# Performance work log

Hardware: AMD Instinct MI355X
Metric: run time of the kernel (lower is better)

Reference implementation:

```python
import jax, jax.numpy as jnp
import numpy as np

ALPHA = 0.2  # LeakyReLU negative slope
MASK_VAL = -9e15


def gat_layer(h, W, a, adj):
    # h: (b, n, f_in); W: (H, f_in, d); a: (H, 2d, 1); adj: (n, n)
    Wh = jnp.einsum('bni,hid->bhnd', h, W)          # (b, H, n, d)
    d = W.shape[-1]
    a1 = a[:, :d, 0]                                # (H, d) -> source term
    a2 = a[:, d:, 0]                                # (H, d) -> target term
    f1 = jnp.einsum('bhnd,hd->bhn', Wh, a1)
    f2 = jnp.einsum('bhnd,hd->bhn', Wh, a2)
    e = jax.nn.leaky_relu(f1[..., :, None] + f2[..., None, :], ALPHA)  # (b, H, n, n)
    e = jnp.where(adj > 0, e, MASK_VAL)
    att = jax.nn.softmax(e, axis=-1)
    out = jnp.einsum('bhij,bhjd->bhid', att, Wh)    # (b, H, n, d)
    b, H, n, dd = out.shape
    # concat heads along feature dim (matches torch.cat(head_outputs, dim=2))
    return jnp.transpose(out, (0, 2, 1, 3)).reshape(b, n, H * dd)


def setup_inputs() -> dict:
    key = jax.random.key(0)
    ks = jax.random.split(key, 8)
    B, N = 131072, 9
    HID, OUT, HEADS = 96, 48, 3
    hd1 = HID // HEADS   # 32
    hd2 = OUT // HEADS   # 16

    def xavier(k, shape, gain=1.414):
        fan_in, fan_out = shape[-2], shape[-1]
        lim = gain * np.sqrt(6.0 / (fan_in + fan_out))
        return jax.random.uniform(k, shape, jnp.float32, -lim, lim)

    obs = jax.random.normal(ks[0], (B, N), dtype=jnp.float32)
    adj = jnp.ones((N, N), dtype=jnp.float32)
    W1 = xavier(ks[1], (HEADS, 1, hd1))
    a1 = xavier(ks[2], (HEADS, 2 * hd1, 1))
    W2 = xavier(ks[3], (HEADS, HID, hd2))
    a2 = xavier(ks[4], (HEADS, 2 * hd2, 1))
    lim = np.sqrt(1.0 / OUT)
    Wp1 = jax.random.uniform(ks[5], (OUT, OUT // 2), jnp.float32, -lim, lim)
    bp1 = jnp.zeros((OUT // 2,), jnp.float32)
    lim2 = np.sqrt(1.0 / (OUT // 2))
    Wp2 = jax.random.uniform(ks[6], (OUT // 2, 1), jnp.float32, -lim2, lim2)
    bp2 = jnp.zeros((1,), jnp.float32)
    return {"obs": obs, "adj": adj, "W1": W1, "a1": a1, "W2": W2, "a2": a2,
            "Wp1": Wp1, "bp1": bp1, "Wp2": Wp2, "bp2": bp2}


def reference(obs, adj, W1, a1, W2, a2, Wp1, bp1, Wp2, bp2):
    h = obs[..., None]                       # (b, n, 1)
    h = jax.nn.elu(gat_layer(h, W1, a1, adj))
    h = gat_layer(h, W2, a2, adj)            # (b, n, output_dim)
    # attention pooling over nodes
    scores = jnp.tanh(h @ Wp1 + bp1) @ Wp2 + bp2   # (b, n, 1)
    w = jax.nn.softmax(scores, axis=1)
    return jnp.sum(w * h, axis=1)            # (b, output_dim)
```

## Files before the change

kernel.cpp:

```cpp
#include <hip/hip_runtime.h>
#include <math.h>

typedef _Float16 h16;
typedef _Float16 v2h __attribute__((ext_vector_type(2)));

#define ALPHA 0.2f
#define MASKV -9000000000000000.0f

constexpr int GSCR = 268;
constexpr int O_S  = 0;
constexpr int O_F1 = 28;
constexpr int O_F2 = 56;
constexpr int O_U  = 92;

#if defined(__has_builtin)
#  if __has_builtin(__builtin_amdgcn_fdot2)
#    define FDOT2(a,b,c) __builtin_amdgcn_fdot2((a),(b),(c),false)
#  endif
#endif
#ifndef FDOT2
__device__ __forceinline__ float fdot2_sw(v2h a, v2h b, float c) {
    return c + (float)a.x*(float)b.x + (float)a.y*(float)b.y;
}
#  define FDOT2(a,b,c) fdot2_sw((a),(b),(c))
#endif

union U4 { float4 f; v2h h[4]; };
union U2 { float2 f; v2h h[2]; };
union U1 { float  f; v2h h;    };

#define WAVE_SYNC() asm volatile("s_waitcnt lgkmcnt(0)" ::: "memory")

__device__ __forceinline__ float fast_rcp(float x) { return __builtin_amdgcn_rcpf(x); }
__device__ __forceinline__ float tanh_fast(float x) {
    float e = __expf(x + x);
    return 1.f - 2.f * fast_rcp(e + 1.f);
}

__global__ void prep_kernel(const float* __restrict__ W2, const float* __restrict__ Wp1,
                            h16* __restrict__ ws) {
    int t = blockIdx.x * 256 + threadIdx.x;
    if (t < 48 * 96) {
        int c = t / 96, i = t - c * 96;
        int h = c >> 4, d = c & 15;
        ws[t] = (h16)W2[(h * 96 + i) * 16 + d];
    } else if (t < 48 * 96 + 576) {
        int t2 = t - 48 * 96;
        int k = t2 / 24, s = t2 - k * 24;
        int l = s / 3, kp = s - 3 * l;
        int clo = l + 16 * kp, chi = clo + 8;
        ws[4608 + 2 * t2]     = (h16)Wp1[clo * 24 + k];
        ws[4608 + 2 * t2 + 1] = (h16)Wp1[chi * 24 + k];
    }
}

__global__ __launch_bounds__(128, 4) void gnn_gat_kernel(
    const float* __restrict__ obs, const float* __restrict__ adj,
    const float* __restrict__ W1,  const float* __restrict__ a1,
    const float* __restrict__ a2,  const float* __restrict__ bp1,
    const float* __restrict__ Wp2, const h16* __restrict__ ws,
    float* __restrict__ out, int B)
{
    __shared__ float sW1[96];
    __shared__ float sC12[6];
    __shared__ unsigned sRb[9];
    __shared__ __align__(16) float smem[16 * GSCR];

    const int tid = threadIdx.x;
    if (tid < 96) sW1[tid] = W1[tid];
    if (tid < 9) {
        unsigned u = 0;
        for (int j = 0; j < 9; ++j)
            u |= (adj[tid * 9 + j] > 0.f ? 1u : 0u) << j;
        sRb[tid] = u;
    }
    if (tid < 6) {
        int gg = tid >> 1, w = tid & 1;
        float s = 0.f;
        for (int d = 0; d < 32; ++d)
            s += W1[gg * 32 + d] * a1[gg * 64 + w * 32 + d];
        sC12[tid] = s;
    }
    __syncthreads();

    const int wv = tid >> 6, lane = tid & 63;
    const int q = lane >> 3, l8 = lane & 7;
    float* g = smem + (wv * 8 + q) * GSCR;
    float4* hUf4 = (float4*)(g + O_U);
    float4* h2f4 = (float4*)g;
    const float4* wsf4 = (const float4*)ws;

    const int slots = gridDim.x * 16;
    for (int b = (blockIdx.x * 2 + wv) * 8 + q; b < B; b += slots) {
        float o_r[9];
        #pragma unroll
        for (int j = 0; j < 9; ++j) o_r[j] = obs[(size_t)b * 9 + j];
        g[O_F1 + l8] = obs[(size_t)b * 9 + l8];
        if (l8 == 0) g[O_F1 + 8] = obs[(size_t)b * 9 + 8];
        WAVE_SYNC();

        #pragma unroll
        for (int it = 0; it < 4; ++it) {
            int t = l8 + 8 * it;
            if (t < 27) {
                int gg = (t >= 18) ? 2 : (t >= 9 ? 1 : 0);
                int n = t - 9 * gg;
                float f1 = sC12[2 * gg] * g[O_F1 + n];
                float c2 = sC12[2 * gg + 1];
                unsigned rbits = sRb[n];
                float e[9], m = -3.0e38f;
                #pragma unroll
                for (int j = 0; j < 9; ++j) {
                    float x = f1 + c2 * o_r[j];
                    x = x > 0.f ? x : ALPHA * x;
                    x = ((rbits >> j) & 1) ? x : MASKV;
                    e[j] = x; m = fmaxf(m, x);
                }
                float sum = 0.f, sw = 0.f;
                #pragma unroll
                for (int j = 0; j < 9; ++j) {
                    float p = __expf(e[j] - m);
                    sum += p; sw += p * o_r[j];
                }
                g[O_S + t] = sw * fast_rcp(sum);
            }
        }
        WAVE_SYNC();

        float acc[9][6];
        #pragma unroll
        for (int n = 0; n < 9; ++n)
            #pragma unroll
            for (int k = 0; k < 6; ++k) acc[n][k] = 0.f;

        for (int p = 0; p < 3; ++p) {
            #pragma unroll
            for (int it = 0; it < 5; ++it) {
                int t = l8 + 8 * it;
                if (t < 36) {
                    int n = t >> 2, ib = t & 3;
                    int i0 = 32 * p + 8 * ib;
                    float sv = g[O_S + p * 9 + n];
                    float4 wa = *(const float4*)&sW1[i0];
                    float4 wb = *(const float4*)&sW1[i0 + 4];
                    float v0 = sv * wa.x, v1 = sv * wa.y, v2 = sv * wa.z, v3 = sv * wa.w;
                    float v4 = sv * wb.x, v5 = sv * wb.y, v6 = sv * wb.z, v7 = sv * wb.w;
                    v0 = v0 > 0.f ? v0 : __expf(v0) - 1.f;
                    v1 = v1 > 0.f ? v1 : __expf(v1) - 1.f;
                    v2 = v2 > 0.f ? v2 : __expf(v2) - 1.f;
                    v3 = v3 > 0.f ? v3 : __expf(v3) - 1.f;
                    v4 = v4 > 0.f ? v4 : __expf(v4) - 1.f;
                    v5 = v5 > 0.f ? v5 : __expf(v5) - 1.f;
                    v6 = v6 > 0.f ? v6 : __expf(v6) - 1.f;
                    v7 = v7 > 0.f ? v7 : __expf(v7) - 1.f;
                    U4 u;
                    u.h[0] = (v2h){(h16)v0, (h16)v1};
                    u.h[1] = (v2h){(h16)v2, (h16)v3};
                    u.h[2] = (v2h){(h16)v4, (h16)v5};
                    u.h[3] = (v2h){(h16)v6, (h16)v7};
                    hUf4[n * 4 + ib] = u.f;
                }
            }
            WAVE_SYNC();

            #pragma unroll
            for (int ib = 0; ib < 4; ++ib) {
                U4 w[6];
                #pragma unroll
                for (int k = 0; k < 6; ++k)
                    w[k].f = wsf4[(l8 + 8 * k) * 12 + p * 4 + ib];
                #pragma unroll
                for (int n = 0; n < 9; ++n) {
                    U4 hh; hh.f = hUf4[n * 4 + ib];
                    #pragma unroll
                    for (int k = 0; k < 6; ++k) {
                        float a = acc[n][k];
                        a = FDOT2(hh.h[0], w[k].h[0], a);
                        a = FDOT2(hh.h[1], w[k].h[1], a);
                        a = FDOT2(hh.h[2], w[k].h[2], a);
                        a = FDOT2(hh.h[3], w[k].h[3], a);
                        acc[n][k] = a;
                    }
                }
            }
            WAVE_SYNC();
        }

        #pragma unroll
        for (int h = 0; h < 3; ++h) {
            float aa0 = a2[h * 32 + l8];
            float aa1 = a2[h * 32 + 8 + l8];
            float ab0 = a2[h * 32 + 16 + l8];
            float ab1 = a2[h * 32 + 24 + l8];
            #pragma unroll
            for (int n = 0; n < 9; ++n) {
                float v1 = acc[n][2 * h] * aa0 + acc[n][2 * h + 1] * aa1;
                float v2 = acc[n][2 * h] * ab0 + acc[n][2 * h + 1] * ab1;
                v1 += __shfl_xor(v1, 1, 8); v1 += __shfl_xor(v1, 2, 8); v1 += __shfl_xor(v1, 4, 8);
                v2 += __shfl_xor(v2, 1, 8); v2 += __shfl_xor(v2, 2, 8); v2 += __shfl_xor(v2, 4, 8);
                if (((h * 9 + n) & 7) == l8) {
                    g[O_F1 + h * 9 + n]  = v1;
                    g[O_F2 + h * 10 + n] = v2;
                }
            }
        }
        WAVE_SYNC();

        #pragma unroll
        for (int it = 0; it < 4; ++it) {
            int t = l8 + 8 * it;
            if (t < 27) {
                int h = (t >= 18) ? 2 : (t >= 9 ? 1 : 0);
                int i = t - 9 * h;
                float f1i = g[O_F1 + t];
                unsigned rbits = sRb[i];
                float e[9], m = -3.0e38f;
                #pragma unroll
                for (int j = 0; j < 9; ++j) {
                    float x = f1i + g[O_F2 + h * 10 + j];
                    x = x > 0.f ? x : ALPHA * x;
                    x = ((rbits >> j) & 1) ? x : MASKV;
                    e[j] = x; m = fmaxf(m, x);
                }
                float p[9], sum = 0.f;
                #pragma unroll
                for (int j = 0; j < 9; ++j) { p[j] = __expf(e[j] - m); sum += p[j]; }
                float r = fast_rcp(sum);
                char* row = (char*)(g + O_U) + t * 24;
                U2 u01, u23; U1 u4;
                u01.h[0] = (v2h){(h16)(p[0] * r), (h16)(p[1] * r)};
                u01.h[1] = (v2h){(h16)(p[2] * r), (h16)(p[3] * r)};
                u23.h[0] = (v2h){(h16)(p[4] * r), (h16)(p[5] * r)};
                u23.h[1] = (v2h){(h16)(p[6] * r), (h16)(p[7] * r)};
                u4.h     = (v2h){(h16)(p[8] * r), (h16)0.f};
                *(float2*)(row)      = u01.f;
                *(float2*)(row + 8)  = u23.f;
                *(float*)(row + 16)  = u4.f;
            }
        }
        WAVE_SYNC();

        #pragma unroll
        for (int h = 0; h < 3; ++h) {
            float t0[9], t1[9];
            #pragma unroll
            for (int i = 0; i < 9; ++i) {
                const char* row = (const char*)(g + O_U) + (h * 9 + i) * 24;
                U2 a01, a23; U1 a4;
                a01.f = *(const float2*)row;
                a23.f = *(const float2*)(row + 8);
                a4.f  = *(const float*)(row + 16);
                float pj[9];
                pj[0] = (float)a01.h[0].x; pj[1] = (float)a01.h[0].y;
                pj[2] = (float)a01.h[1].x; pj[3] = (float)a01.h[1].y;
                pj[4] = (float)a23.h[0].x; pj[5] = (float)a23.h[0].y;
                pj[6] = (float)a23.h[1].x; pj[7] = (float)a23.h[1].y;
                pj[8] = (float)a4.h.x;
                float s0 = 0.f, s1 = 0.f;
                #pragma unroll
                for (int j = 0; j < 9; ++j) {
                    s0 += pj[j] * acc[j][2 * h];
                    s1 += pj[j] * acc[j][2 * h + 1];
                }
                t0[i] = s0; t1[i] = s1;
            }
            #pragma unroll
            for (int i = 0; i < 9; ++i) { acc[i][2 * h] = t0[i]; acc[i][2 * h + 1] = t1[i]; }
        }

        #pragma unroll
        for (int n = 0; n < 9; ++n) {
            #pragma unroll
            for (int kp = 0; kp < 3; ++kp) {
                U1 u; u.h = (v2h){(h16)acc[n][2 * kp], (h16)acc[n][2 * kp + 1]};
                ((float*)g)[n * 24 + 3 * l8 + kp] = u.f;
            }
        }
        WAVE_SYNC();

        float sp[9];
        #pragma unroll
        for (int n = 0; n < 9; ++n) sp[n] = 0.f;
        #pragma unroll
        for (int kk = 0; kk < 3; ++kk) {
            int k = l8 + 8 * kk;
            float wqv = Wp2[k];
            float bqv = bp1[k];
            U4 w0, w1, w2u, w3, w4, w5;
            w0.f = wsf4[576 + k * 6 + 0];
            w1.f = wsf4[576 + k * 6 + 1];
            w2u.f = wsf4[576 + k * 6 + 2];
            w3.f = wsf4[576 + k * 6 + 3];
            w4.f = wsf4[576 + k * 6 + 4];
            w5.f = wsf4[576 + k * 6 + 5];
            #pragma unroll
            for (int n = 0; n < 9; ++n) {
                float a = 0.f;
                U4 x;
                x.f = h2f4[n * 6 + 0];
                a = FDOT2(x.h[0], w0.h[0], a); a = FDOT2(x.h[1], w0.h[1], a);
                a = FDOT2(x.h[2], w0.h[2], a); a = FDOT2(x.h[3], w0.h[3], a);
                x.f = h2f4[n * 6 + 1];
                a = FDOT2(x.h[0], w1.h[0], a); a = FDOT2(x.h[1], w1.h[1], a);
                a = FDOT2(x.h[2], w1.h[2], a); a = FDOT2(x.h[3], w1.h[3], a);
                x.f = h2f4[n * 6 + 2];
                a = FDOT2(x.h[0], w2u.h[0], a); a = FDOT2(x.h[1], w2u.h[1], a);
                a = FDOT2(x.h[2], w2u.h[2], a); a = FDOT2(x.h[3], w2u.h[3], a);
                x.f = h2f4[n * 6 + 3];
                a = FDOT2(x.h[0], w3.h[0], a); a = FDOT2(x.h[1], w3.h[1], a);
                a = FDOT2(x.h[2], w3.h[2], a); a = FDOT2(x.h[3], w3.h[3], a);
                x.f = h2f4[n * 6 + 4];
                a = FDOT2(x.h[0], w4.h[0], a); a = FDOT2(x.h[1], w4.h[1], a);
                a = FDOT2(x.h[2], w4.h[2], a); a = FDOT2(x.h[3], w4.h[3], a);
                x.f = h2f4[n * 6 + 5];
                a = FDOT2(x.h[0], w5.h[0], a); a = FDOT2(x.h[1], w5.h[1], a);
                a = FDOT2(x.h[2], w5.h[2], a); a = FDOT2(x.h[3], w5.h[3], a);
                float tv = tanh_fast(a + bqv);
                sp[n] += tv * wqv;
            }
        }
        #pragma unroll
        for (int n = 0; n < 9; ++n) {
            sp[n] += __shfl_xor(sp[n], 1, 8);
            sp[n] += __shfl_xor(sp[n], 2, 8);
            sp[n] += __shfl_xor(sp[n], 4, 8);
        }

        float mx = sp[0];
        #pragma unroll
        for (int n = 1; n < 9; ++n) mx = fmaxf(mx, sp[n]);
        float wn9[9], sum = 0.f;
        #pragma unroll
        for (int n = 0; n < 9; ++n) { wn9[n] = __expf(sp[n] - mx); sum += wn9[n]; }
        float r = fast_rcp(sum);
        #pragma unroll
        for (int k = 0; k < 6; ++k) {
            float ov = 0.f;
            #pragma unroll
            for (int n = 0; n < 9; ++n) ov += wn9[n] * acc[n][k];
            out[(size_t)b * 48 + l8 + 8 * k] = ov * r;
        }
        WAVE_SYNC();
    }
}

extern "C" void kernel_launch(void* const* d_in, const int* in_sizes, int n_in,
                              void* d_out, int out_size, void* d_ws, size_t ws_size,
                              hipStream_t stream) {
    const float* obs = (const float*)d_in[0];
    const float* adj = (const float*)d_in[1];
    const float* W1  = (const float*)d_in[2];
    const float* a1  = (const float*)d_in[3];
    const float* W2  = (const float*)d_in[4];
    const float* a2  = (const float*)d_in[5];
    const float* Wp1 = (const float*)d_in[6];
    const float* bp1 = (const float*)d_in[7];
    const float* Wp2 = (const float*)d_in[8];
    float* out = (float*)d_out;
    h16* ws = (h16*)d_ws;

    const int B = in_sizes[0] / 9;

    prep_kernel<<<(48 * 96 + 576 + 255) / 256, 256, 0, stream>>>(W2, Wp1, ws);

    gnn_gat_kernel<<<4096, 128, 0, stream>>>(
        obs, adj, W1, a1, a2, bp1, Wp2, ws, out, B);
}
```

Before: 338.0 us.

## Replace fdot2 second-layer GEMM with MFMA 16x16x32 f16 matrix cores

The per-lane fdot2 accumulation for the layer-2 projection (9 nodes x 96 inputs x 48 outputs per sample) is replaced by MFMA 16x16x32 f16 instructions. Each wave packs the 8 samples' 72 rows into a shared A tile, padded to 80 rows. Results go back through shared memory so the existing per-lane acc layout is rebuilt for the later stages. Occupancy hint drops from 4 to 2 blocks per CU, and the change adds LDS traffic, extra syncs, and wasted padded rows.

```diff
diff --git a/kernel.cpp b/kernel.cpp
--- a/kernel.cpp
+++ b/kernel.cpp
@@ -2,7 +2,9 @@
 #include <math.h>
 
 typedef _Float16 h16;
-typedef _Float16 v2h __attribute__((ext_vector_type(2)));
+typedef _Float16 v2h  __attribute__((ext_vector_type(2)));
+typedef _Float16 f16x8 __attribute__((ext_vector_type(8)));
+typedef float    f32x4 __attribute__((ext_vector_type(4)));
 
 #define ALPHA 0.2f
 #define MASKV -9000000000000000.0f
@@ -12,6 +14,7 @@
 constexpr int O_F1 = 28;
 constexpr int O_F2 = 56;
 constexpr int O_U  = 92;
+constexpr int CBS  = 19;
 
 #if defined(__has_builtin)
 #  if __has_builtin(__builtin_amdgcn_fdot2)
@@ -54,7 +57,7 @@
     }
 }
 
-__global__ __launch_bounds__(128, 4) void gnn_gat_kernel(
+__global__ __launch_bounds__(128, 2) void gnn_gat_kernel(
     const float* __restrict__ obs, const float* __restrict__ adj,
     const float* __restrict__ W1,  const float* __restrict__ a1,
     const float* __restrict__ a2,  const float* __restrict__ bp1,
@@ -65,6 +68,7 @@
     __shared__ float sC12[6];
     __shared__ unsigned sRb[9];
     __shared__ __align__(16) float smem[16 * GSCR];
+    __shared__ __align__(16) h16 sA[2][80][40];
 
     const int tid = threadIdx.x;
     if (tid < 96) sW1[tid] = W1[tid];
@@ -85,8 +89,10 @@
 
     const int wv = tid >> 6, lane = tid & 63;
     const int q = lane >> 3, l8 = lane & 7;
-    float* g = smem + (wv * 8 + q) * GSCR;
-    float4* hUf4 = (float4*)(g + O_U);
+    const int lm = lane & 15, lg = lane >> 4;
+    float* g  = smem + (wv * 8 + q) * GSCR;
+    float* cb = smem + wv * 8 * GSCR;
+    h16 (*A)[40] = sA[wv];
     float4* h2f4 = (float4*)g;
     const float4* wsf4 = (const float4*)ws;
 
@@ -127,11 +133,12 @@
         }
         WAVE_SYNC();
 
-        float acc[9][6];
-        #pragma unroll
-        for (int n = 0; n < 9; ++n)
-            #pragma unroll
-            for (int k = 0; k < 6; ++k) acc[n][k] = 0.f;
+        f32x4 cfr[5][3];
+        #pragma unroll
+        for (int mt = 0; mt < 5; ++mt)
+            #pragma unroll
+            for (int nt = 0; nt < 3; ++nt)
+                cfr[mt][nt] = (f32x4){0.f, 0.f, 0.f, 0.f};
 
         for (int p = 0; p < 3; ++p) {
             #pragma unroll
@@ -158,30 +165,45 @@
                     u.h[1] = (v2h){(h16)v2, (h16)v3};
                     u.h[2] = (v2h){(h16)v4, (h16)v5};
                     u.h[3] = (v2h){(h16)v6, (h16)v7};
-                    hUf4[n * 4 + ib] = u.f;
+                    *(float4*)&A[9 * q + n][8 * ib] = u.f;
                 }
             }
             WAVE_SYNC();
 
-            #pragma unroll
-            for (int ib = 0; ib < 4; ++ib) {
-                U4 w[6];
-                #pragma unroll
-                for (int k = 0; k < 6; ++k)
-                    w[k].f = wsf4[(l8 + 8 * k) * 12 + p * 4 + ib];
-                #pragma unroll
-                for (int n = 0; n < 9; ++n) {
-                    U4 hh; hh.f = hUf4[n * 4 + ib];
-                    #pragma unroll
-                    for (int k = 0; k < 6; ++k) {
-                        float a = acc[n][k];
-                        a = FDOT2(hh.h[0], w[k].h[0], a);
-                        a = FDOT2(hh.h[1], w[k].h[1], a);
-                        a = FDOT2(hh.h[2], w[k].h[2], a);
-                        a = FDOT2(hh.h[3], w[k].h[3], a);
-                        acc[n][k] = a;
-                    }
-                }
+            f16x8 af[5];
+            #pragma unroll
+            for (int mt = 0; mt < 5; ++mt)
+                af[mt] = *(const f16x8*)&A[16 * mt + lm][8 * lg];
+
+            #pragma unroll
+            for (int nt = 0; nt < 3; ++nt) {
+                f16x8 bf = *(const f16x8*)(ws + (16 * nt + lm) * 96 + 32 * p + 8 * lg);
+                #pragma unroll
+                for (int mt = 0; mt < 5; ++mt)
+                    cfr[mt][nt] = __builtin_amdgcn_mfma_f32_16x16x32_f16(
+                        af[mt], bf, cfr[mt][nt], 0, 0, 0);
+            }
+            WAVE_SYNC();
+        }
+
+        float acc[9][6];
+        #pragma unroll
+        for (int nt = 0; nt < 3; ++nt) {
+            #pragma unroll
+            for (int mt = 0; mt < 5; ++mt) {
+                int rbase = 16 * mt + 4 * lg;
+                #pragma unroll
+                for (int r = 0; r < 4; ++r) {
+                    int row = rbase + r;
+                    if (row < 72) cb[row * CBS + lm] = cfr[mt][nt][r];
+                }
+            }
+            WAVE_SYNC();
+            #pragma unroll
+            for (int n = 0; n < 9; ++n) {
+                int ad = (9 * q + n) * CBS + l8;
+                acc[n][2 * nt]     = cb[ad];
+                acc[n][2 * nt + 1] = cb[ad + 8];
             }
             WAVE_SYNC();
         }
```

New measurement: 809.0 us. 2.39x slower.
